# Kernel optimization log

Hardware: AMD Instinct MI355X
Metric: run time of the kernel (lower is better)

The kernel has to match this reference:

```python
import jax, jax.numpy as jnp
import numpy as np

D = 1024        # number of Hawkes dimensions (N_g * K)
M = 32768       # number of events
BETA = 1.0      # fixed exponential-kernel decay
T_MAX = 1000    # observation horizon
EPS_MU = 1e-06
EPS_LOG = 1e-08


def setup_inputs() -> dict:
    key = jax.random.key(0)
    k1, k2, k3, k4 = jax.random.split(key, 4)
    t_events = jnp.sort(jax.random.uniform(k1, (M,), dtype=jnp.float32) * T_MAX)
    marks = jax.random.randint(k2, (M,), 0, D)
    # learned params around the torch init (-3 / -4) with a little noise
    log_mu = jnp.full((D,), -3.0, dtype=jnp.float32) + 0.1 * jax.random.normal(k3, (D,), dtype=jnp.float32)
    log_alpha = jnp.full((D, D), -4.0, dtype=jnp.float32) + 0.1 * jax.random.normal(k4, (D, D), dtype=jnp.float32)
    return {"t_events": t_events, "marks": marks, "log_mu": log_mu,
            "log_alpha": log_alpha, "T_max": T_MAX}


def reference(t_events, marks, log_mu, log_alpha, T_max):
    """Hawkes log-likelihood; faithful translation of XuHawkesTorch.intensity_loglik."""
    mu = jax.nn.softplus(log_mu) + EPS_MU          # [D]
    alpha = jax.nn.softplus(log_alpha)             # [D, D]
    T_max = jnp.asarray(T_max, dtype=t_events.dtype)

    # inter-event gaps; dt[0] = 0 so first event sees no decay (matches torch loop)
    dt = jnp.diff(t_events, prepend=t_events[:1])  # [M]
    decay = jnp.exp(-BETA * dt)                    # [M]

    def step(S, inp):
        dec, d = inp
        S = dec * S                                # exp-decay of excitation state
        lam_d = mu[d] + alpha[d] @ S               # intensity at event d
        ll = jnp.log(lam_d + EPS_LOG)
        S = S.at[d].add(1.0)                       # event adds unit excitation
        return S, ll

    S0 = jnp.zeros((D,), dtype=t_events.dtype)
    _, lls = jax.lax.scan(step, S0, (decay, marks))

    # compensator integral over [0, T_max]
    one_minus_exp = 1.0 - jnp.exp(-BETA * (T_max - t_events))   # [M]
    contrib = jax.ops.segment_sum(one_minus_exp, marks, num_segments=D)  # [D]
    integral = mu * T_max + alpha @ (contrib / BETA)            # [D]

    return lls.sum() - integral.sum()
```

## Files before the change

kernel.cpp:

```cpp
#include <hip/hip_runtime.h>


#define D 1024
#define M 32768
#define C 64
#define NC (M / C)
#define NB (NC * 8)
#define NG 16
#define GC (NC / NG)
#define TMAXV 1000.0f
#define EPSMU 1e-6f
#define EPSLOG 1e-8f

__device__ __forceinline__ float softplus(float x) {
    return (x > 0.0f) ? (x + log1pf(__expf(-x))) : log1pf(__expf(x));
}

__device__ __forceinline__ unsigned short f2bf(float x) {
    unsigned u = __float_as_uint(x);
    return (unsigned short)((u + 0x7FFFu + ((u >> 16) & 1u)) >> 16);
}
__device__ __forceinline__ float bf2f(unsigned short h) {
    return __uint_as_float(((unsigned)h) << 16);
}

__global__ void k1(const float* __restrict__ t_ev, const int* __restrict__ marks,
                   const float* __restrict__ log_alpha, const float* __restrict__ log_mu,
                   unsigned short* __restrict__ ab, float* __restrict__ mu,
                   float* __restrict__ P, float* __restrict__ Sl, float* __restrict__ A) {
    __shared__ float Lh[GC * 256];
    __shared__ float dec[GC];
    __shared__ float tns[GC];
    int t = threadIdx.x;
    int b = blockIdx.x;

    if (b < 256) {
        int r0 = b * 4;
        float4 cs = {0.f, 0.f, 0.f, 0.f};
        for (int r = 0; r < 4; ++r) {
            const float4* src = (const float4*)(log_alpha + (size_t)(r0 + r) * D);
            float4 v = src[t];
            float4 a;
            a.x = softplus(v.x);
            a.y = softplus(v.y);
            a.z = softplus(v.z);
            a.w = softplus(v.w);
            cs.x += a.x; cs.y += a.y; cs.z += a.z; cs.w += a.w;
            ushort4 h;
            h.x = f2bf(a.x); h.y = f2bf(a.y); h.z = f2bf(a.z); h.w = f2bf(a.w);
            ((ushort4*)(ab + (size_t)(r0 + r) * D))[t] = h;
        }
        ((float4*)(P + (size_t)b * D))[t] = cs;
    } else if (b == 256) {
#pragma unroll
        for (int q = 0; q < 4; ++q) {
            int k = t + 256 * q;
            mu[k] = softplus(log_mu[k]) + EPSMU;
        }
    } else {
        int fb = b - 257;
        int g = fb >> 2, db = fb & 3;
#pragma unroll
        for (int q = 0; q < GC; ++q) Lh[q * 256 + t] = 0.0f;
        if (t < GC) {
            int gc = g * GC + t;
            float tn = (gc + 1 < NC) ? t_ev[(gc + 1) * C] : t_ev[M - 1];
            tns[t] = tn;
            dec[t] = (gc + 1 < NC) ? __expf(t_ev[gc * C] - tn) : 1.0f;
        }
        __syncthreads();
        int base = g * (GC * C);
#pragma unroll
        for (int it = 0; it < 8; ++it) {
            int e = it * 256 + t;
            float te = t_ev[base + e];
            int m = marks[base + e];
            int lc = e >> 6;
            int ml = m - db * 256;
            if ((unsigned)ml < 256u) atomicAdd(&Lh[lc * 256 + ml], __expf(te - tns[lc]));
        }
        __syncthreads();
        int k = db * 256 + t;
        float S = 0.0f;
        for (int lc = 0; lc < GC; ++lc) {
            Sl[(size_t)(g * GC + lc) * D + k] = S;
            S = S * dec[lc] + Lh[lc * 256 + t];
        }
        A[(size_t)g * D + k] = S;
    }
}

__global__ void k_mid(const float* __restrict__ P, float* __restrict__ colsum,
                      const float* __restrict__ t_ev, const float* __restrict__ A,
                      float* __restrict__ Sg, float* __restrict__ cumdec) {
    int t = threadIdx.x;
    if (blockIdx.x < 8) {
        __shared__ float red[8][128];
        int colL = t & 127, seg = t >> 7;
        int col = blockIdx.x * 128 + colL;
        float s = 0.0f;
#pragma unroll
        for (int j = 0; j < 32; ++j)
            s += P[(size_t)(seg * 32 + j) * D + col];
        red[seg][colL] = s;
        __syncthreads();
        if (t < 128) {
            float v = 0.0f;
#pragma unroll
            for (int k = 0; k < 8; ++k) v += red[k][t];
            colsum[blockIdx.x * 128 + t] = v;
        }
    } else {
        __shared__ float dec[NC];
        __shared__ float Pg[NG];
        if (t < NC)
            dec[t] = (t + 1 < NC) ? __expf(t_ev[t * C] - t_ev[(t + 1) * C]) : 1.0f;
        __syncthreads();
        if (t < NC) {
            int g = t >> 5, r = t & 31;
            float p = 1.0f;
            for (int j = 0; j < r; ++j) p *= dec[g * GC + j];
            cumdec[t] = p;
            if (r == GC - 1) Pg[g] = p * dec[t];
        }
        __syncthreads();
        float a[NG];
#pragma unroll
        for (int g2 = 0; g2 < NG; ++g2) a[g2] = A[(size_t)g2 * D + t];
        float S = 0.0f;
#pragma unroll
        for (int g2 = 0; g2 < NG; ++g2) {
            Sg[(size_t)g2 * D + t] = S;
            S = S * Pg[g2] + a[g2];
        }
    }
}

__launch_bounds__(256)
__global__ void k_main(const float* __restrict__ t_ev, const int* __restrict__ marks,
                       const unsigned short* __restrict__ ab, const float* __restrict__ mu,
                       const float* __restrict__ colsum, const float* __restrict__ Sl,
                       const float* __restrict__ Sg, const float* __restrict__ cumdec,
                       float* __restrict__ llp, float* __restrict__ compp) {
    __shared__ float S_lds[D];
    __shared__ float t_lds[C];
    __shared__ int d_lds[C];
    __shared__ float red[8];
    int t = threadIdx.x;
    int c = blockIdx.x >> 3, sub = blockIdx.x & 7;
    int g = c >> 5;
    float cd = cumdec[c];
#pragma unroll
    for (int q = 0; q < 4; ++q) {
        int k = t + 256 * q;
        S_lds[k] = Sl[(size_t)c * D + k] + Sg[(size_t)g * D + k] * cd;
    }
    if (t < C) {
        t_lds[t] = t_ev[c * C + t];
        d_lds[t] = marks[c * C + t];
    }
    __syncthreads();
    int wave = t >> 6, lane = t & 63;
    float t0 = t_lds[0];
    float ll_acc = 0.0f, comp_acc = 0.0f;
#pragma unroll
    for (int i = sub * 8 + wave; i < sub * 8 + 8; i += 4) {
        int row = d_lds[i];
        float ti = t_lds[i];
        float mu_r = mu[row];
        float cs_r = colsum[row];
        const uint4* arow = (const uint4*)(ab + (size_t)row * D);
        float acc_dot = 0.0f;
#pragma unroll
        for (int u = 0; u < 2; ++u) {
            uint4 pk = arow[2 * lane + u];
            const float4* sp = (const float4*)(S_lds + 16 * lane + 8 * u);
            float4 s0 = sp[0], s1 = sp[1];
            acc_dot += __uint_as_float(pk.x << 16) * s0.x
                     + __uint_as_float(pk.x & 0xFFFF0000u) * s0.y
                     + __uint_as_float(pk.y << 16) * s0.z
                     + __uint_as_float(pk.y & 0xFFFF0000u) * s0.w
                     + __uint_as_float(pk.z << 16) * s1.x
                     + __uint_as_float(pk.z & 0xFFFF0000u) * s1.y
                     + __uint_as_float(pk.w << 16) * s1.z
                     + __uint_as_float(pk.w & 0xFFFF0000u) * s1.w;
        }
        float part = acc_dot * __expf(t0 - ti);
        if (lane < i) {
            part += bf2f(ab[(size_t)row * D + d_lds[lane]]) * __expf(t_lds[lane] - ti);
        }
#pragma unroll
        for (int off = 32; off > 0; off >>= 1) part += __shfl_xor(part, off);
        if (lane == 0) {
            ll_acc += __logf(mu_r + part + EPSLOG);
            comp_acc += cs_r * (1.0f - __expf(ti - TMAXV));
        }
    }
    if (lane == 0) {
        red[wave] = ll_acc;
        red[4 + wave] = comp_acc;
    }
    __syncthreads();
    if (t == 0) {
        llp[blockIdx.x] = red[0] + red[1] + red[2] + red[3];
        compp[blockIdx.x] = red[4] + red[5] + red[6] + red[7];
    }
}

__global__ void k_final(const float* __restrict__ llp, const float* __restrict__ compp,
                        const float* __restrict__ mu, float* __restrict__ out) {
    __shared__ float r_ll[1024], r_cm[1024], r_mu[1024];
    int t = threadIdx.x;
    float sll = 0.0f, scm = 0.0f;
#pragma unroll
    for (int j = 0; j < 4; ++j) {
        sll += llp[t + 1024 * j];
        scm += compp[t + 1024 * j];
    }
    r_ll[t] = sll;
    r_cm[t] = scm;
    r_mu[t] = mu[t];
    __syncthreads();
    for (int off = 512; off > 0; off >>= 1) {
        if (t < off) {
            r_ll[t] += r_ll[t + off];
            r_cm[t] += r_cm[t + off];
            r_mu[t] += r_mu[t + off];
        }
        __syncthreads();
    }
    if (t == 0) out[0] = r_ll[0] - (TMAXV * r_mu[0] + r_cm[0]);
}

extern "C" void kernel_launch(void* const* d_in, const int* in_sizes, int n_in,
                              void* d_out, int out_size, void* d_ws, size_t ws_size,
                              hipStream_t stream) {
    const float* t_ev = (const float*)d_in[0];
    const int* marks = (const int*)d_in[1];
    const float* log_mu = (const float*)d_in[2];
    const float* log_alpha = (const float*)d_in[3];
    float* out = (float*)d_out;

    float* w = (float*)d_ws;
    unsigned short* ab = (unsigned short*)w;
    float* Sl = w + (size_t)D * D / 2;
    float* mu = Sl + (size_t)NC * D;
    float* colsum = mu + D;
    float* P = colsum + D;
    float* llp = P + (size_t)256 * D;
    float* compp = llp + NB;
    float* A = compp + NB;
    float* Sg = A + (size_t)NG * D;
    float* cumdec = Sg + (size_t)NG * D;

    k1<<<321, 256, 0, stream>>>(t_ev, marks, log_alpha, log_mu, ab, mu, P, Sl, A);
    k_mid<<<9, 1024, 0, stream>>>(P, colsum, t_ev, A, Sg, cumdec);
    k_main<<<NB, 256, 0, stream>>>(t_ev, marks, ab, mu, colsum, Sl, Sg, cumdec, llp, compp);
    k_final<<<1, 1024, 0, stream>>>(llp, compp, mu, out);
}
```

Before: 88.96 us.

## Process a whole chunk per block with 512 threads and simplify final reduction

k_main previously launched 8 blocks per 64-event chunk, and each block rebuilt the same 1024-entry state vector in LDS from Sl and Sg. It now launches one 512-thread block per chunk, so each wave handles 8 events and the state is built once per chunk with float4 loads. This cuts redundant global reads and LDS setup by a factor of eight, at the cost of fewer blocks (512) and lower parallelism per event. The final reduction now uses wave shuffles over 512 partials instead of an LDS tree over 4096.

```diff
diff --git a/kernel.cpp b/kernel.cpp
--- a/kernel.cpp
+++ b/kernel.cpp
@@ -5,7 +5,6 @@
 #define M 32768
 #define C 64
 #define NC (M / C)
-#define NB (NC * 8)
 #define NG 16
 #define GC (NC / NG)
 #define TMAXV 1000.0f
@@ -136,7 +135,7 @@
     }
 }
 
-__launch_bounds__(256)
+__launch_bounds__(512)
 __global__ void k_main(const float* __restrict__ t_ev, const int* __restrict__ marks,
                        const unsigned short* __restrict__ ab, const float* __restrict__ mu,
                        const float* __restrict__ colsum, const float* __restrict__ Sl,
@@ -145,26 +144,34 @@
     __shared__ float S_lds[D];
     __shared__ float t_lds[C];
     __shared__ int d_lds[C];
-    __shared__ float red[8];
-    int t = threadIdx.x;
-    int c = blockIdx.x >> 3, sub = blockIdx.x & 7;
+    __shared__ float red_ll[8], red_cm[8];
+    int t = threadIdx.x;
+    int c = blockIdx.x;
     int g = c >> 5;
     float cd = cumdec[c];
-#pragma unroll
-    for (int q = 0; q < 4; ++q) {
-        int k = t + 256 * q;
-        S_lds[k] = Sl[(size_t)c * D + k] + Sg[(size_t)g * D + k] * cd;
-    }
-    if (t < C) {
-        t_lds[t] = t_ev[c * C + t];
-        d_lds[t] = marks[c * C + t];
+    if (t < 256) {
+        float4 a = ((const float4*)(Sl + (size_t)c * D))[t];
+        float4 b = ((const float4*)(Sg + (size_t)g * D))[t];
+        float4 s;
+        s.x = a.x + b.x * cd;
+        s.y = a.y + b.y * cd;
+        s.z = a.z + b.z * cd;
+        s.w = a.w + b.w * cd;
+        ((float4*)S_lds)[t] = s;
+    } else if (t < 320) {
+        int e = t - 256;
+        t_lds[e] = t_ev[c * C + e];
+    } else if (t < 384) {
+        int e = t - 320;
+        d_lds[e] = marks[c * C + e];
     }
     __syncthreads();
     int wave = t >> 6, lane = t & 63;
     float t0 = t_lds[0];
     float ll_acc = 0.0f, comp_acc = 0.0f;
 #pragma unroll
-    for (int i = sub * 8 + wave; i < sub * 8 + 8; i += 4) {
+    for (int k = 0; k < 8; ++k) {
+        int i = wave * 8 + k;
         int row = d_lds[i];
         float ti = t_lds[i];
         float mu_r = mu[row];
@@ -197,39 +204,36 @@
         }
     }
     if (lane == 0) {
-        red[wave] = ll_acc;
-        red[4 + wave] = comp_acc;
+        red_ll[wave] = ll_acc;
+        red_cm[wave] = comp_acc;
     }
     __syncthreads();
     if (t == 0) {
-        llp[blockIdx.x] = red[0] + red[1] + red[2] + red[3];
-        compp[blockIdx.x] = red[4] + red[5] + red[6] + red[7];
+        float a = 0.0f, b = 0.0f;
+#pragma unroll
+        for (int w = 0; w < 8; ++w) { a += red_ll[w]; b += red_cm[w]; }
+        llp[c] = a;
+        compp[c] = b;
     }
 }
 
 __global__ void k_final(const float* __restrict__ llp, const float* __restrict__ compp,
                         const float* __restrict__ mu, float* __restrict__ out) {
-    __shared__ float r_ll[1024], r_cm[1024], r_mu[1024];
-    int t = threadIdx.x;
-    float sll = 0.0f, scm = 0.0f;
-#pragma unroll
-    for (int j = 0; j < 4; ++j) {
-        sll += llp[t + 1024 * j];
-        scm += compp[t + 1024 * j];
-    }
-    r_ll[t] = sll;
-    r_cm[t] = scm;
-    r_mu[t] = mu[t];
+    __shared__ float acc[16];
+    int t = threadIdx.x;
+    float x = -TMAXV * mu[t];
+    if (t < NC) x += llp[t] - compp[t];
+#pragma unroll
+    for (int off = 32; off > 0; off >>= 1) x += __shfl_xor(x, off);
+    int wave = t >> 6, lane = t & 63;
+    if (lane == 0) acc[wave] = x;
     __syncthreads();
-    for (int off = 512; off > 0; off >>= 1) {
-        if (t < off) {
-            r_ll[t] += r_ll[t + off];
-            r_cm[t] += r_cm[t + off];
-            r_mu[t] += r_mu[t + off];
-        }
-        __syncthreads();
-    }
-    if (t == 0) out[0] = r_ll[0] - (TMAXV * r_mu[0] + r_cm[0]);
+    if (t < 16) {
+        float v = acc[t];
+#pragma unroll
+        for (int off = 8; off > 0; off >>= 1) v += __shfl_xor(v, off, 16);
+        if (t == 0) out[0] = v;
+    }
 }
 
 extern "C" void kernel_launch(void* const* d_in, const int* in_sizes, int n_in,
@@ -248,13 +252,13 @@
     float* colsum = mu + D;
     float* P = colsum + D;
     float* llp = P + (size_t)256 * D;
-    float* compp = llp + NB;
-    float* A = compp + NB;
+    float* compp = llp + NC;
+    float* A = compp + NC;
     float* Sg = A + (size_t)NG * D;
     float* cumdec = Sg + (size_t)NG * D;
 
     k1<<<321, 256, 0, stream>>>(t_ev, marks, log_alpha, log_mu, ab, mu, P, Sl, A);
     k_mid<<<9, 1024, 0, stream>>>(P, colsum, t_ev, A, Sg, cumdec);
-    k_main<<<NB, 256, 0, stream>>>(t_ev, marks, ab, mu, colsum, Sl, Sg, cumdec, llp, compp);
+    k_main<<<NC, 512, 0, stream>>>(t_ev, marks, ab, mu, colsum, Sl, Sg, cumdec, llp, compp);
     k_final<<<1, 1024, 0, stream>>>(llp, compp, mu, out);
 }
```

Measured after the change: 89.26 us. No clear change (+0.3%).
